# Kernel tuning notes

Measured on AMD Instinct MI355X. Metric: run time of the kernel, lower is better.

The kernel has to match this reference:

```python
import jax, jax.numpy as jnp
import numpy as np

N_TOKENS = 32768
D_MODEL = 1024
TOT_EXPERT = 16
TOP_K = 2


def setup_inputs() -> dict:
    key = jax.random.key(0)
    k1, k2 = jax.random.split(key)
    inp = jax.random.normal(k1, (N_TOKENS, D_MODEL), dtype=jnp.float32)
    # nn.Linear(d_model, tot_expert, bias=False) weight: [tot_expert, d_model]
    W = jax.random.normal(k2, (TOT_EXPERT, D_MODEL), dtype=jnp.float32) * 0.02
    return {"inp": inp, "W": W}


def reference(inp, W):
    # gate logits: [N, E]
    logits = jnp.einsum('nd,ed->ne', inp, W)
    # top-k over experts (sorted order differs from torch sorted=False, but the
    # selected set and the downstream math are identical)
    top_k_logits, top_k_indices = jax.lax.top_k(logits, TOP_K)  # [N, K]
    # scatter top-k logits into a -inf buffer, then softmax over experts
    rows = jnp.arange(inp.shape[0])[:, None]
    router = jnp.full_like(logits, -jnp.inf).at[rows, top_k_indices].set(top_k_logits)
    router_probs = jax.nn.softmax(router, axis=-1)  # [N, E]
    # load-balance loss: f_i (no-grad expert selection freq) dot P_i (mean prob)
    f_i = jnp.zeros((TOT_EXPERT,), jnp.float32).at[top_k_indices.reshape(-1)].add(1.0) / inp.shape[0]
    P_i = jnp.mean(router_probs.astype(jnp.float32), axis=0)
    loss = jnp.sum(jax.lax.stop_gradient(f_i) * P_i) * TOT_EXPERT
    # gather the softmaxed scores of the selected experts
    top_k_scores = jnp.take_along_axis(router_probs, top_k_indices, axis=-1)  # [N, K]
    return top_k_indices, top_k_scores, loss
```

## Files before the change

### kernel.cpp

```cpp
#include <hip/hip_runtime.h>
#include <math.h>

#define N_TOKENS 32768
#define D_MODEL  1024
#define N_EXPERT 16
#define T        16
#define NBLK     (N_TOKENS / T)

typedef float f32x4 __attribute__((ext_vector_type(4)));
typedef float f32x2 __attribute__((ext_vector_type(2)));

template<int CTRL>
static __device__ __forceinline__ float dpp_xor(float v) {
    return __int_as_float(__builtin_amdgcn_update_dpp(
        0, __float_as_int(v), CTRL, 0xF, 0xF, true));
}

static __device__ __forceinline__ float dot4pk(f32x4 x, f32x4 w) {
    f32x2 xl = __builtin_shufflevector(x, x, 0, 1);
    f32x2 xh = __builtin_shufflevector(x, x, 2, 3);
    f32x2 wl = __builtin_shufflevector(w, w, 0, 1);
    f32x2 wh = __builtin_shufflevector(w, w, 2, 3);
    f32x2 m, r;
    asm("v_pk_mul_f32 %0, %1, %2" : "=v"(m) : "v"(xl), "v"(wl));
    asm("v_pk_fma_f32 %0, %1, %2, %3" : "=v"(r) : "v"(xh), "v"(wh), "v"(m));
    return r.x + r.y;
}


__global__ __launch_bounds__(256, 3)
void gate_kernel(const float* __restrict__ inp,
                 const float* __restrict__ W,
                 float* __restrict__ out,
                 float* __restrict__ ws)
{
    const int tid  = threadIdx.x;
    const int wave = tid >> 6;
    const int lane = tid & 63;
    const int d0   = wave * 256 + lane * 4;
    const int tok0 = blockIdx.x * T;
    const bool hi8 = (lane & 8) != 0;
    const bool hi4 = (lane & 4) != 0;
    const bool hi2 = (lane & 2) != 0;
    const bool hi1 = (lane & 1) != 0;

    f32x4 wreg[N_EXPERT];
    #pragma unroll
    for (int e = 0; e < N_EXPERT; ++e)
        wreg[e] = *reinterpret_cast<const f32x4*>(W + e * D_MODEL + d0);

    __shared__ float lds_part[T][4][N_EXPERT];
    __shared__ float lds_cnt[T][N_EXPERT];
    __shared__ float lds_ps[T][N_EXPERT];

    const float* xptr = inp + (size_t)tok0 * D_MODEL + d0;

#define LOADX(xr, t) xr = *reinterpret_cast<const f32x4*>(xptr + (t) * D_MODEL);

#define DOTOK(xv, t) do { \
    float a0 =dot4pk(xv,wreg[0]),  a1 =dot4pk(xv,wreg[1]);  \
    float a2 =dot4pk(xv,wreg[2]),  a3 =dot4pk(xv,wreg[3]);  \
    float a4 =dot4pk(xv,wreg[4]),  a5 =dot4pk(xv,wreg[5]);  \
    float a6 =dot4pk(xv,wreg[6]),  a7 =dot4pk(xv,wreg[7]);  \
    float a8 =dot4pk(xv,wreg[8]),  a9 =dot4pk(xv,wreg[9]);  \
    float a10=dot4pk(xv,wreg[10]), a11=dot4pk(xv,wreg[11]); \
    float a12=dot4pk(xv,wreg[12]), a13=dot4pk(xv,wreg[13]); \
    float a14=dot4pk(xv,wreg[14]), a15=dot4pk(xv,wreg[15]); \
    float b0 = (hi8 ? a8  : a0) + dpp_xor<0x128>(hi8 ? a0 : a8 ); \
    float b1 = (hi8 ? a9  : a1) + dpp_xor<0x128>(hi8 ? a1 : a9 ); \
    float b2 = (hi8 ? a10 : a2) + dpp_xor<0x128>(hi8 ? a2 : a10); \
    float b3 = (hi8 ? a11 : a3) + dpp_xor<0x128>(hi8 ? a3 : a11); \
    float b4 = (hi8 ? a12 : a4) + dpp_xor<0x128>(hi8 ? a4 : a12); \
    float b5 = (hi8 ? a13 : a5) + dpp_xor<0x128>(hi8 ? a5 : a13); \
    float b6 = (hi8 ? a14 : a6) + dpp_xor<0x128>(hi8 ? a6 : a14); \
    float b7 = (hi8 ? a15 : a7) + dpp_xor<0x128>(hi8 ? a7 : a15); \
    float c0 = (hi4 ? b4 : b0) + __shfl_xor(hi4 ? b0 : b4, 4); \
    float c1 = (hi4 ? b5 : b1) + __shfl_xor(hi4 ? b1 : b5, 4); \
    float c2 = (hi4 ? b6 : b2) + __shfl_xor(hi4 ? b2 : b6, 4); \
    float c3 = (hi4 ? b7 : b3) + __shfl_xor(hi4 ? b3 : b7, 4); \
    float e0 = (hi2 ? c2 : c0) + dpp_xor<0x4E>(hi2 ? c0 : c2); \
    float e1 = (hi2 ? c3 : c1) + dpp_xor<0x4E>(hi2 ? c1 : c3); \
    float s0 = (hi1 ? e1 : e0) + dpp_xor<0xB1>(hi1 ? e0 : e1); \
    s0 += __shfl_xor(s0, 16); \
    s0 += __shfl_xor(s0, 32); \
    if (lane < N_EXPERT) lds_part[t][wave][lane] = s0; \
} while (0)

    f32x4 x0, x1, x2, x3;
    LOADX(x0, 0) LOADX(x1, 1) LOADX(x2, 2) LOADX(x3, 3)
    for (int g = 0; g < 3; ++g) {
        const int tb = g * 4;
        DOTOK(x0, tb + 0); LOADX(x0, tb + 4)
        DOTOK(x1, tb + 1); LOADX(x1, tb + 5)
        DOTOK(x2, tb + 2); LOADX(x2, tb + 6)
        DOTOK(x3, tb + 3); LOADX(x3, tb + 7)
    }
    DOTOK(x0, 12); DOTOK(x1, 13); DOTOK(x2, 14); DOTOK(x3, 15);

    __syncthreads();

    {
        const int tgrp = tid >> 4;
        const int el   = tid & 15;
        float v1 = lds_part[tgrp][0][el] + lds_part[tgrp][1][el]
                 + lds_part[tgrp][2][el] + lds_part[tgrp][3][el];
        int   i1 = el;
        float v2 = -INFINITY;
        int   i2 = 0;
        #pragma unroll
        for (int m = 1; m <= 8; m <<= 1) {
            float o1 = __shfl_xor(v1, m);
            int  oi1 = __shfl_xor(i1, m);
            float o2 = __shfl_xor(v2, m);
            int  oi2 = __shfl_xor(i2, m);
            bool afirst = (v1 > o1) || (v1 == o1 && i1 < oi1);
            float c1v = afirst ? v1 : o1;   int c1i = afirst ? i1 : oi1;
            float bv  = afirst ? o1 : v1;   int bi  = afirst ? oi1 : i1;
            float sv  = afirst ? v2 : o2;   int si  = afirst ? i2 : oi2;
            bool sgt  = (bv > sv) || (bv == sv && bi < si);
            v1 = c1v; i1 = c1i;
            v2 = sgt ? bv : sv;  i2 = sgt ? bi : si;
        }
        float tt = expf(v2 - v1);
        float p1 = 1.f / (1.f + tt);
        float p2 = tt * p1;
        const int tok = tok0 + tgrp;
        if (el == 0) {
            *reinterpret_cast<float2*>(out + 2 * tok) =
                make_float2((float)i1, (float)i2);
            *reinterpret_cast<float2*>(out + 2 * N_TOKENS + 2 * tok) =
                make_float2(p1, p2);
        }
        lds_cnt[tgrp][el] = (el == i1 ? 1.f : 0.f) + (el == i2 ? 1.f : 0.f);
        lds_ps [tgrp][el] = (el == i1 ? p1 : 0.f) + (el == i2 ? p2 : 0.f);
    }
    __syncthreads();

    if (tid < 32) {
        const int el = tid & 15;
        float ssum = 0.f;
        if (tid < 16) {
            #pragma unroll
            for (int g = 0; g < T; ++g) ssum += lds_cnt[g][el];
        } else {
            #pragma unroll
            for (int g = 0; g < T; ++g) ssum += lds_ps[g][el];
        }
        ws[blockIdx.x * 32 + tid] = ssum;
    }
#undef LOADX
#undef DOTOK
}

__global__ void loss_kernel(const float* __restrict__ ws, float* __restrict__ out)
{
    __shared__ float partial[8][32];
    __shared__ float col[32];
    const int tid = threadIdx.x;
    const int c   = tid & 31;
    const int ch  = tid >> 5;
    float s = 0.f;
    for (int b = 0; b < NBLK / 8; ++b)
        s += ws[(size_t)(ch * (NBLK / 8) + b) * 32 + c];
    partial[ch][c] = s;
    __syncthreads();
    if (tid < 32) {
        float t = 0.f;
        #pragma unroll
        for (int k = 0; k < 8; ++k) t += partial[k][tid];
        col[tid] = t;
    }
    __syncthreads();
    if (tid == 0) {
        float sum = 0.f;
        #pragma unroll
        for (int e = 0; e < N_EXPERT; ++e)
            sum += col[e] * col[16 + e];
        out[4 * N_TOKENS] = sum * (float)N_EXPERT
                          / ((float)N_TOKENS * (float)N_TOKENS);
    }
}

extern "C" void kernel_launch(void* const* d_in, const int* in_sizes, int n_in,
                              void* d_out, int out_size, void* d_ws, size_t ws_size,
                              hipStream_t stream)
{
    const float* inp = (const float*)d_in[0];
    const float* W   = (const float*)d_in[1];
    float* out = (float*)d_out;
    float* ws  = (float*)d_ws;

    gate_kernel<<<NBLK, 256, 0, stream>>>(inp, W, out, ws);
    loss_kernel<<<1, 256, 0, stream>>>(ws, out);
}
```

Before: 42.71 us.

## Process 64 tokens per block with lane-permuted weights and register-accumulated stats

Each block now loops over four batches of 16 tokens, for 64 tokens per block, so 512 blocks run instead of 2048. The weight registers are loaded once per block and reused across more tokens. The weight rows are permuted per lane (expert j^p), which removes the lane-dependent selects from the butterfly transpose-reduction. Per-expert count and probability sums are kept in registers across batches and reduced once at the end, so the loss kernel reads fewer partials, and its loop is unrolled with four accumulators. The cost is fewer blocks to spread latency over and an extra sync per batch, with LDS double-buffered by batch parity.

```diff
diff --git a/kernel.cpp b/kernel.cpp
--- a/kernel.cpp
+++ b/kernel.cpp
@@ -4,8 +4,10 @@
 #define N_TOKENS 32768
 #define D_MODEL  1024
 #define N_EXPERT 16
-#define T        16
-#define NBLK     (N_TOKENS / T)
+#define TPB      256
+#define NBLK     512
+#define TOKS     64
+#define BATCH    16
 
 typedef float f32x4 __attribute__((ext_vector_type(4)));
 typedef float f32x2 __attribute__((ext_vector_type(2)));
@@ -37,27 +39,24 @@
     const int tid  = threadIdx.x;
     const int wave = tid >> 6;
     const int lane = tid & 63;
+    const int p    = lane & 15;
     const int d0   = wave * 256 + lane * 4;
-    const int tok0 = blockIdx.x * T;
-    const bool hi8 = (lane & 8) != 0;
-    const bool hi4 = (lane & 4) != 0;
-    const bool hi2 = (lane & 2) != 0;
-    const bool hi1 = (lane & 1) != 0;
+    const int base = blockIdx.x * TOKS;
 
     f32x4 wreg[N_EXPERT];
     #pragma unroll
-    for (int e = 0; e < N_EXPERT; ++e)
-        wreg[e] = *reinterpret_cast<const f32x4*>(W + e * D_MODEL + d0);
-
-    __shared__ float lds_part[T][4][N_EXPERT];
-    __shared__ float lds_cnt[T][N_EXPERT];
-    __shared__ float lds_ps[T][N_EXPERT];
-
-    const float* xptr = inp + (size_t)tok0 * D_MODEL + d0;
+    for (int j = 0; j < N_EXPERT; ++j)
+        wreg[j] = *reinterpret_cast<const f32x4*>(W + (j ^ p) * D_MODEL + d0);
+
+    __shared__ float lds_part[2][BATCH][4][N_EXPERT];
+    __shared__ float lds_red[4][2][N_EXPERT];
+
+    float cnt_acc = 0.f;
+    float ps_acc  = 0.f;
 
 #define LOADX(xr, t) xr = *reinterpret_cast<const f32x4*>(xptr + (t) * D_MODEL);
 
-#define DOTOK(xv, t) do { \
+#define DOTOK(xv, t, BUF) do { \
     float a0 =dot4pk(xv,wreg[0]),  a1 =dot4pk(xv,wreg[1]);  \
     float a2 =dot4pk(xv,wreg[2]),  a3 =dot4pk(xv,wreg[3]);  \
     float a4 =dot4pk(xv,wreg[4]),  a5 =dot4pk(xv,wreg[5]);  \
@@ -66,87 +65,95 @@
     float a10=dot4pk(xv,wreg[10]), a11=dot4pk(xv,wreg[11]); \
     float a12=dot4pk(xv,wreg[12]), a13=dot4pk(xv,wreg[13]); \
     float a14=dot4pk(xv,wreg[14]), a15=dot4pk(xv,wreg[15]); \
-    float b0 = (hi8 ? a8  : a0) + dpp_xor<0x128>(hi8 ? a0 : a8 ); \
-    float b1 = (hi8 ? a9  : a1) + dpp_xor<0x128>(hi8 ? a1 : a9 ); \
-    float b2 = (hi8 ? a10 : a2) + dpp_xor<0x128>(hi8 ? a2 : a10); \
-    float b3 = (hi8 ? a11 : a3) + dpp_xor<0x128>(hi8 ? a3 : a11); \
-    float b4 = (hi8 ? a12 : a4) + dpp_xor<0x128>(hi8 ? a4 : a12); \
-    float b5 = (hi8 ? a13 : a5) + dpp_xor<0x128>(hi8 ? a5 : a13); \
-    float b6 = (hi8 ? a14 : a6) + dpp_xor<0x128>(hi8 ? a6 : a14); \
-    float b7 = (hi8 ? a15 : a7) + dpp_xor<0x128>(hi8 ? a7 : a15); \
-    float c0 = (hi4 ? b4 : b0) + __shfl_xor(hi4 ? b0 : b4, 4); \
-    float c1 = (hi4 ? b5 : b1) + __shfl_xor(hi4 ? b1 : b5, 4); \
-    float c2 = (hi4 ? b6 : b2) + __shfl_xor(hi4 ? b2 : b6, 4); \
-    float c3 = (hi4 ? b7 : b3) + __shfl_xor(hi4 ? b3 : b7, 4); \
-    float e0 = (hi2 ? c2 : c0) + dpp_xor<0x4E>(hi2 ? c0 : c2); \
-    float e1 = (hi2 ? c3 : c1) + dpp_xor<0x4E>(hi2 ? c1 : c3); \
-    float s0 = (hi1 ? e1 : e0) + dpp_xor<0xB1>(hi1 ? e0 : e1); \
+    float b0 = a0 + dpp_xor<0x128>(a8);  \
+    float b1 = a1 + dpp_xor<0x128>(a9);  \
+    float b2 = a2 + dpp_xor<0x128>(a10); \
+    float b3 = a3 + dpp_xor<0x128>(a11); \
+    float b4 = a4 + dpp_xor<0x128>(a12); \
+    float b5 = a5 + dpp_xor<0x128>(a13); \
+    float b6 = a6 + dpp_xor<0x128>(a14); \
+    float b7 = a7 + dpp_xor<0x128>(a15); \
+    float c0 = b0 + __shfl_xor(b4, 4); \
+    float c1 = b1 + __shfl_xor(b5, 4); \
+    float c2 = b2 + __shfl_xor(b6, 4); \
+    float c3 = b3 + __shfl_xor(b7, 4); \
+    float d0_ = c0 + dpp_xor<0x4E>(c2); \
+    float d1_ = c1 + dpp_xor<0x4E>(c3); \
+    float s0  = d0_ + dpp_xor<0xB1>(d1_); \
     s0 += __shfl_xor(s0, 16); \
     s0 += __shfl_xor(s0, 32); \
-    if (lane < N_EXPERT) lds_part[t][wave][lane] = s0; \
+    if (lane < N_EXPERT) BUF[t][wave][lane] = s0; \
 } while (0)
 
-    f32x4 x0, x1, x2, x3;
-    LOADX(x0, 0) LOADX(x1, 1) LOADX(x2, 2) LOADX(x3, 3)
-    for (int g = 0; g < 3; ++g) {
-        const int tb = g * 4;
-        DOTOK(x0, tb + 0); LOADX(x0, tb + 4)
-        DOTOK(x1, tb + 1); LOADX(x1, tb + 5)
-        DOTOK(x2, tb + 2); LOADX(x2, tb + 6)
-        DOTOK(x3, tb + 3); LOADX(x3, tb + 7)
-    }
-    DOTOK(x0, 12); DOTOK(x1, 13); DOTOK(x2, 14); DOTOK(x3, 15);
-
+    for (int b = 0; b < TOKS / BATCH; ++b) {
+        const int tb0 = base + b * BATCH;
+        const float* xptr = inp + (size_t)tb0 * D_MODEL + d0;
+        float (*buf)[4][N_EXPERT] = lds_part[b & 1];
+
+        f32x4 x0, x1, x2, x3;
+        LOADX(x0, 0) LOADX(x1, 1) LOADX(x2, 2) LOADX(x3, 3)
+        for (int g = 0; g < 3; ++g) {
+            const int t = g * 4;
+            DOTOK(x0, t + 0, buf); LOADX(x0, t + 4)
+            DOTOK(x1, t + 1, buf); LOADX(x1, t + 5)
+            DOTOK(x2, t + 2, buf); LOADX(x2, t + 6)
+            DOTOK(x3, t + 3, buf); LOADX(x3, t + 7)
+        }
+        DOTOK(x0, 12, buf); DOTOK(x1, 13, buf);
+        DOTOK(x2, 14, buf); DOTOK(x3, 15, buf);
+
+        __syncthreads();
+
+        {
+            const int tgrp = tid >> 4;
+            const int el   = tid & 15;
+            float v1 = buf[tgrp][0][el] + buf[tgrp][1][el]
+                     + buf[tgrp][2][el] + buf[tgrp][3][el];
+            int   i1 = el;
+            float v2 = -INFINITY;
+            int   i2 = 0;
+            #pragma unroll
+            for (int m = 1; m <= 8; m <<= 1) {
+                float o1 = __shfl_xor(v1, m);
+                int  oi1 = __shfl_xor(i1, m);
+                float o2 = __shfl_xor(v2, m);
+                int  oi2 = __shfl_xor(i2, m);
+                bool afirst = (v1 > o1) || (v1 == o1 && i1 < oi1);
+                float c1v = afirst ? v1 : o1;   int c1i = afirst ? i1 : oi1;
+                float bv  = afirst ? o1 : v1;   int bi  = afirst ? oi1 : i1;
+                float sv  = afirst ? v2 : o2;   int si  = afirst ? i2 : oi2;
+                bool sgt  = (bv > sv) || (bv == sv && bi < si);
+                v1 = c1v; i1 = c1i;
+                v2 = sgt ? bv : sv;  i2 = sgt ? bi : si;
+            }
+            float tt = expf(v2 - v1);
+            float p1 = 1.f / (1.f + tt);
+            float p2 = tt * p1;
+            const int tok = tb0 + tgrp;
+            if (el == 0) {
+                *reinterpret_cast<float2*>(out + 2 * tok) =
+                    make_float2((float)i1, (float)i2);
+                *reinterpret_cast<float2*>(out + 2 * N_TOKENS + 2 * tok) =
+                    make_float2(p1, p2);
+            }
+            cnt_acc += (el == i1 ? 1.f : 0.f) + (el == i2 ? 1.f : 0.f);
+            ps_acc  += (el == i1 ? p1  : 0.f) + (el == i2 ? p2  : 0.f);
+        }
+    }
+
+    cnt_acc += __shfl_xor(cnt_acc, 16); cnt_acc += __shfl_xor(cnt_acc, 32);
+    ps_acc  += __shfl_xor(ps_acc, 16);  ps_acc  += __shfl_xor(ps_acc, 32);
+    if (lane < N_EXPERT) {
+        lds_red[wave][0][lane] = cnt_acc;
+        lds_red[wave][1][lane] = ps_acc;
+    }
     __syncthreads();
-
-    {
-        const int tgrp = tid >> 4;
-        const int el   = tid & 15;
-        float v1 = lds_part[tgrp][0][el] + lds_part[tgrp][1][el]
-                 + lds_part[tgrp][2][el] + lds_part[tgrp][3][el];
-        int   i1 = el;
-        float v2 = -INFINITY;
-        int   i2 = 0;
-        #pragma unroll
-        for (int m = 1; m <= 8; m <<= 1) {
-            float o1 = __shfl_xor(v1, m);
-            int  oi1 = __shfl_xor(i1, m);
-            float o2 = __shfl_xor(v2, m);
-            int  oi2 = __shfl_xor(i2, m);
-            bool afirst = (v1 > o1) || (v1 == o1 && i1 < oi1);
-            float c1v = afirst ? v1 : o1;   int c1i = afirst ? i1 : oi1;
-            float bv  = afirst ? o1 : v1;   int bi  = afirst ? oi1 : i1;
-            float sv  = afirst ? v2 : o2;   int si  = afirst ? i2 : oi2;
-            bool sgt  = (bv > sv) || (bv == sv && bi < si);
-            v1 = c1v; i1 = c1i;
-            v2 = sgt ? bv : sv;  i2 = sgt ? bi : si;
-        }
-        float tt = expf(v2 - v1);
-        float p1 = 1.f / (1.f + tt);
-        float p2 = tt * p1;
-        const int tok = tok0 + tgrp;
-        if (el == 0) {
-            *reinterpret_cast<float2*>(out + 2 * tok) =
-                make_float2((float)i1, (float)i2);
-            *reinterpret_cast<float2*>(out + 2 * N_TOKENS + 2 * tok) =
-                make_float2(p1, p2);
-        }
-        lds_cnt[tgrp][el] = (el == i1 ? 1.f : 0.f) + (el == i2 ? 1.f : 0.f);
-        lds_ps [tgrp][el] = (el == i1 ? p1 : 0.f) + (el == i2 ? p2 : 0.f);
-    }
-    __syncthreads();
-
     if (tid < 32) {
         const int el = tid & 15;
-        float ssum = 0.f;
-        if (tid < 16) {
-            #pragma unroll
-            for (int g = 0; g < T; ++g) ssum += lds_cnt[g][el];
-        } else {
-            #pragma unroll
-            for (int g = 0; g < T; ++g) ssum += lds_ps[g][el];
-        }
-        ws[blockIdx.x * 32 + tid] = ssum;
+        const int which = tid >> 4;
+        float v = lds_red[0][which][el] + lds_red[1][which][el]
+                + lds_red[2][which][el] + lds_red[3][which][el];
+        ws[blockIdx.x * 32 + tid] = v;
     }
 #undef LOADX
 #undef DOTOK
@@ -159,10 +166,14 @@
     const int tid = threadIdx.x;
     const int c   = tid & 31;
     const int ch  = tid >> 5;
-    float s = 0.f;
-    for (int b = 0; b < NBLK / 8; ++b)
-        s += ws[(size_t)(ch * (NBLK / 8) + b) * 32 + c];
-    partial[ch][c] = s;
+    float s0 = 0.f, s1 = 0.f, s2 = 0.f, s3 = 0.f;
+    for (int b = 0; b < NBLK / 8; b += 4) {
+        s0 += ws[(size_t)(ch * (NBLK / 8) + b + 0) * 32 + c];
+        s1 += ws[(size_t)(ch * (NBLK / 8) + b + 1) * 32 + c];
+        s2 += ws[(size_t)(ch * (NBLK / 8) + b + 2) * 32 + c];
+        s3 += ws[(size_t)(ch * (NBLK / 8) + b + 3) * 32 + c];
+    }
+    partial[ch][c] = (s0 + s1) + (s2 + s3);
     __syncthreads();
     if (tid < 32) {
         float t = 0.f;
@@ -190,6 +201,6 @@
     float* out = (float*)d_out;
     float* ws  = (float*)d_ws;
 
-    gate_kernel<<<NBLK, 256, 0, stream>>>(inp, W, out, ws);
+    gate_kernel<<<NBLK, TPB, 0, stream>>>(inp, W, out, ws);
     loss_kernel<<<1, 256, 0, stream>>>(ws, out);
 }
```

Result: faster. 39.01 us (-8.7%).
